# Kernel tuning notes

Measured on AMD Instinct MI355X. Metric: run time of the kernel, lower is better.

The kernel has to match this reference:

```python
import jax, jax.numpy as jnp
import numpy as np

B, N, E, H = 8, 2048, 768, 8
D = E // H  # head dim = 96


def setup_inputs() -> dict:
    key = jax.random.key(0)
    ks = jax.random.split(key, 9)
    s = 0.02
    return {
        "x": jax.random.normal(ks[0], (B, N, E), dtype=jnp.float32),
        "Wq": jax.random.normal(ks[1], (E, E), dtype=jnp.float32) * s,
        "bq": jax.random.normal(ks[2], (E,), dtype=jnp.float32) * s,
        "Wk": jax.random.normal(ks[3], (E, E), dtype=jnp.float32) * s,
        "bk": jax.random.normal(ks[4], (E,), dtype=jnp.float32) * s,
        "Wv": jax.random.normal(ks[5], (E, E), dtype=jnp.float32) * s,
        "bv": jax.random.normal(ks[6], (E,), dtype=jnp.float32) * s,
        "Wo": jax.random.normal(ks[7], (E, E), dtype=jnp.float32) * s,
        "bo": jax.random.normal(ks[8], (E,), dtype=jnp.float32) * s,
    }


def _split_heads(t):
    # [b, n, (h d)] -> [b, h, n, d]
    b, n, e = t.shape
    return t.reshape(b, n, H, D).transpose(0, 2, 1, 3)


def reference(x, Wq, bq, Wk, bk, Wv, bv, Wo, bo):
    q = _split_heads(x @ Wq + bq)
    k = _split_heads(x @ Wk + bk)
    v = _split_heads(x @ Wv + bv)
    energy = jnp.einsum("bhqd,bhkd->bhqk", q, k)
    # Faithful quirk of the source: softmax first, THEN divide by sqrt(emb_size)
    att = jax.nn.softmax(energy, axis=-1) / jnp.sqrt(jnp.float32(E))
    out = jnp.einsum("bhqk,bhkd->bhqd", att, v)
    out = out.transpose(0, 2, 1, 3).reshape(x.shape[0], x.shape[1], E)
    return out @ Wo + bo
```

## Files before the change

kernel.cpp:

```cpp
#include <hip/hip_runtime.h>
#include <hip/hip_bf16.h>
#include <stdint.h>

#define BATCH 8
#define NSEQ  2048
#define EMB   768
#define NH    8
#define HD    96

typedef unsigned short u16;
typedef __attribute__((ext_vector_type(8))) short short8;
typedef __attribute__((ext_vector_type(4))) float f32x4;
typedef __attribute__((ext_vector_type(16))) float f32x16;

static __device__ __forceinline__ u16 f2bf(float f) {
  union { float f; uint32_t u; } c{f};
  uint32_t u = c.u;
  return (u16)((u + 0x7FFFu + ((u >> 16) & 1u)) >> 16);
}

__global__ __launch_bounds__(256) void k_convert_x(const float* __restrict__ x,
                                                   u16* __restrict__ xb) {
  size_t i = ((size_t)blockIdx.x * 256 + threadIdx.x) * 8;
  float4 a = *(const float4*)(x + i);
  float4 b = *(const float4*)(x + i + 4);
  short8 o;
  o[0] = f2bf(a.x); o[1] = f2bf(a.y); o[2] = f2bf(a.z); o[3] = f2bf(a.w);
  o[4] = f2bf(b.x); o[5] = f2bf(b.y); o[6] = f2bf(b.z); o[7] = f2bf(b.w);
  *(short8*)(xb + i) = o;
}

__global__ __launch_bounds__(256) void k_wtrans(const float* __restrict__ Wq,
                                                const float* __restrict__ Wk,
                                                const float* __restrict__ Wv,
                                                const float* __restrict__ Wo,
                                                u16* __restrict__ WTall) {
  int z = blockIdx.z;
  const float* W = (z == 0) ? Wq : (z == 1) ? Wk : (z == 2) ? Wv : Wo;
  u16* WT = WTall + (size_t)z * EMB * EMB;
  __shared__ float tile[32][33];
  int o0 = blockIdx.x * 32, i0 = blockIdx.y * 32;
  int tx = threadIdx.x, ty = threadIdx.y;
#pragma unroll
  for (int r = 0; r < 4; ++r)
    tile[ty * 4 + r][tx] = W[(size_t)(i0 + ty * 4 + r) * EMB + o0 + tx];
  __syncthreads();
#pragma unroll
  for (int r = 0; r < 4; ++r)
    WT[(size_t)(o0 + ty * 4 + r) * EMB + i0 + tx] = f2bf(tile[tx][ty * 4 + r]);
}

template <bool OUTF32>
static __device__ __forceinline__ void gemm_body(const u16* __restrict__ A,
                                                 const u16* __restrict__ WT,
                                                 const float* __restrict__ bias,
                                                 void* __restrict__ out,
                                                 int m0, int n0, float oscale) {
  __shared__ u16 As[128 * 64];
  __shared__ u16 Bs[128 * 64];
  const int t = threadIdx.x;
  const int w = t >> 6, l = t & 63;
  const int lr = l & 15, lg = l >> 4;
  const int wm = (w >> 1) * 64, wn = (w & 1) * 64;
  f32x4 acc[4][4] = {};
  for (int kt = 0; kt < 12; ++kt) {
    const int k0 = kt * 64;
#pragma unroll
    for (int i = 0; i < 4; ++i) {
      int g = (w * 4 + i) * 64 + l;
      int m = g >> 3, k8 = (g & 7) * 8;
      const u16* sa = A + (size_t)(m0 + m) * EMB + k0 + k8;
      __builtin_amdgcn_global_load_lds((const __attribute__((address_space(1))) void*)sa,
                                       (__attribute__((address_space(3))) void*)&As[(w * 4 + i) * 512],
                                       16, 0, 0);
      const u16* sb = WT + (size_t)(n0 + m) * EMB + k0 + k8;
      __builtin_amdgcn_global_load_lds((const __attribute__((address_space(1))) void*)sb,
                                       (__attribute__((address_space(3))) void*)&Bs[(w * 4 + i) * 512],
                                       16, 0, 0);
    }
    __syncthreads();
#pragma unroll
    for (int ks = 0; ks < 2; ++ks) {
      short8 af[4], bfr[4];
#pragma unroll
      for (int mf = 0; mf < 4; ++mf)
        af[mf] = *(const short8*)&As[(wm + mf * 16 + lr) * 64 + ks * 32 + lg * 8];
#pragma unroll
      for (int nf = 0; nf < 4; ++nf)
        bfr[nf] = *(const short8*)&Bs[(wn + nf * 16 + lr) * 64 + ks * 32 + lg * 8];
#pragma unroll
      for (int mf = 0; mf < 4; ++mf)
#pragma unroll
        for (int nf = 0; nf < 4; ++nf)
          acc[mf][nf] = __builtin_amdgcn_mfma_f32_16x16x32_bf16(af[mf], bfr[nf], acc[mf][nf], 0, 0, 0);
    }
    __syncthreads();
  }
#pragma unroll
  for (int nf = 0; nf < 4; ++nf) {
    int col = n0 + wn + nf * 16 + lr;
    float bv = bias[col];
#pragma unroll
    for (int mf = 0; mf < 4; ++mf)
#pragma unroll
      for (int r = 0; r < 4; ++r) {
        int row = m0 + wm + mf * 16 + lg * 4 + r;
        float v = (acc[mf][nf][r] + bv) * oscale;
        if (OUTF32)
          ((float*)out)[(size_t)row * EMB + col] = v;
        else
          ((u16*)out)[(size_t)row * EMB + col] = f2bf(v);
      }
  }
}

__global__ __launch_bounds__(256) void k_qkv_gemm(const u16* __restrict__ X,
                                                  const u16* __restrict__ WTall,
                                                  const float* __restrict__ bq,
                                                  const float* __restrict__ bk,
                                                  const float* __restrict__ bv,
                                                  u16* __restrict__ Q, u16* __restrict__ K,
                                                  u16* __restrict__ V) {
  int z = blockIdx.z;
  const u16* WT = WTall + (size_t)z * EMB * EMB;
  const float* bias = (z == 0) ? bq : (z == 1) ? bk : bv;
  u16* out = (z == 0) ? Q : (z == 1) ? K : V;
  float sc = (z == 0) ? 1.4426950408889634f : 1.0f;
  gemm_body<false>(X, WT, bias, out, blockIdx.x * 128, blockIdx.y * 128, sc);
}

__global__ __launch_bounds__(256) void k_out_gemm(const u16* __restrict__ AO,
                                                  const u16* __restrict__ WTo,
                                                  const float* __restrict__ bo,
                                                  float* __restrict__ out) {
  gemm_body<true>(AO, WTo, bo, out, blockIdx.x * 128, blockIdx.y * 128, 1.0f);
}

__global__ __launch_bounds__(256) void k_vtrans(const u16* __restrict__ V,
                                                u16* __restrict__ VT) {
  const int bh = blockIdx.y, b = bh >> 3, h = bh & 7;
  const int n0 = blockIdx.x * 128;
  __shared__ u16 LT[96][136];
  const int t = threadIdx.x;
#pragma unroll
  for (int i = 0; i < 6; ++i) {
    int c = i * 256 + t;
    int n = c / 12, d8 = (c % 12) * 8;
    short8 v = *(const short8*)(V + ((size_t)(b * NSEQ + n0 + n)) * EMB + h * HD + d8);
#pragma unroll
    for (int j = 0; j < 8; ++j) LT[d8 + j][n] = (u16)v[j];
  }
  __syncthreads();
#pragma unroll
  for (int i = 0; i < 6; ++i) {
    int c = i * 256 + t;
    int d = c / 16, n8 = (c % 16) * 8;
    short8 v = *(const short8*)&LT[d][n8];
    *(short8*)(VT + ((size_t)bh * HD + d) * NSEQ + n0 + n8) = v;
  }
}

__global__ __launch_bounds__(256) void k_attn(const u16* __restrict__ Q,
                                              const u16* __restrict__ K,
                                              const u16* __restrict__ VT,
                                              u16* __restrict__ AO) {
  __shared__ u16 Ks[64][104];
  __shared__ u16 Vs[96][72];
  const int t = threadIdx.x, w = t >> 6, l = t & 63;
  const int l31 = l & 31, hi = l >> 5;
  const int bh = blockIdx.y, b = bh >> 3, h = bh & 7;
  const int q0 = blockIdx.x * 128 + w * 32;
  const size_t rowBase = (size_t)b * NSEQ;

  short8 qf[6];
#pragma unroll
  for (int ksd = 0; ksd < 6; ++ksd)
    qf[ksd] = *(const short8*)(Q + (rowBase + q0 + l31) * EMB + h * HD + ksd * 16 + hi * 8);

  f32x16 oacc[3] = {};
  float ls0 = 0.f, ls1 = 0.f, ls2 = 0.f, ls3 = 0.f;

  short8 kr[3], vr[3];
  auto load_tile = [&](int kv0) {
#pragma unroll
    for (int i = 0; i < 3; ++i) {
      int c = i * 256 + t;
      int kn = c / 12, kd8 = (c % 12) * 8;
      kr[i] = *(const short8*)(K + (rowBase + kv0 + kn) * EMB + h * HD + kd8);
      int vd = c / 8, vn8 = (c % 8) * 8;
      vr[i] = *(const short8*)(VT + ((size_t)bh * HD + vd) * NSEQ + kv0 + vn8);
    }
  };
  auto write_tile = [&]() {
#pragma unroll
    for (int i = 0; i < 3; ++i) {
      int c = i * 256 + t;
      int kn = c / 12, kd8 = (c % 12) * 8;
      *(short8*)&Ks[kn][kd8] = kr[i];
      int vd = c / 8, vn8 = (c % 8) * 8;
      *(short8*)&Vs[vd][vn8] = vr[i];
    }
  };
  load_tile(0);
  write_tile();
  __syncthreads();

  for (int tt = 0; tt < 32; ++tt) {
    if (tt < 31) load_tile((tt + 1) * 64);

    f32x16 s0 = {}, s1 = {};
    __builtin_amdgcn_s_setprio(1);
#pragma unroll
    for (int ksd = 0; ksd < 6; ++ksd) {
      short8 kf0 = *(const short8*)&Ks[l31][ksd * 16 + hi * 8];
      short8 kf1 = *(const short8*)&Ks[32 + l31][ksd * 16 + hi * 8];
      s0 = __builtin_amdgcn_mfma_f32_32x32x16_bf16(kf0, qf[ksd], s0, 0, 0, 0);
      s1 = __builtin_amdgcn_mfma_f32_32x32x16_bf16(kf1, qf[ksd], s1, 0, 0, 0);
    }
    __builtin_amdgcn_s_setprio(0);

#pragma unroll
    for (int i = 0; i < 16; i += 4) {
      float e0, e1, e2, e3, f0, f1, f2, f3;
      asm("v_exp_f32 %0, %1" : "=v"(e0) : "v"(s0[i + 0]));
      asm("v_exp_f32 %0, %1" : "=v"(e1) : "v"(s0[i + 1]));
      asm("v_exp_f32 %0, %1" : "=v"(e2) : "v"(s0[i + 2]));
      asm("v_exp_f32 %0, %1" : "=v"(e3) : "v"(s0[i + 3]));
      asm("v_exp_f32 %0, %1" : "=v"(f0) : "v"(s1[i + 0]));
      asm("v_exp_f32 %0, %1" : "=v"(f1) : "v"(s1[i + 1]));
      asm("v_exp_f32 %0, %1" : "=v"(f2) : "v"(s1[i + 2]));
      asm("v_exp_f32 %0, %1" : "=v"(f3) : "v"(s1[i + 3]));
      s0[i + 0] = e0; s0[i + 1] = e1; s0[i + 2] = e2; s0[i + 3] = e3;
      s1[i + 0] = f0; s1[i + 1] = f1; s1[i + 2] = f2; s1[i + 3] = f3;
      ls0 += e0 + e1; ls1 += e2 + e3;
      ls2 += f0 + f1; ls3 += f2 + f3;
    }

    short8 pa[4];
#pragma unroll
    for (int mt = 0; mt < 2; ++mt) {
#pragma unroll
      for (int kp = 0; kp < 2; ++kp) {
        const int rb = kp * 8;
        uint32_t w0, w1, w2, w3;
        if (mt == 0) {
          asm("v_cvt_pk_bf16_f32 %0, %1, %2" : "=v"(w0) : "v"(s0[rb + 0]), "v"(s0[rb + 1]));
          asm("v_cvt_pk_bf16_f32 %0, %1, %2" : "=v"(w1) : "v"(s0[rb + 2]), "v"(s0[rb + 3]));
          asm("v_cvt_pk_bf16_f32 %0, %1, %2" : "=v"(w2) : "v"(s0[rb + 4]), "v"(s0[rb + 5]));
          asm("v_cvt_pk_bf16_f32 %0, %1, %2" : "=v"(w3) : "v"(s0[rb + 6]), "v"(s0[rb + 7]));
        } else {
          asm("v_cvt_pk_bf16_f32 %0, %1, %2" : "=v"(w0) : "v"(s1[rb + 0]), "v"(s1[rb + 1]));
          asm("v_cvt_pk_bf16_f32 %0, %1, %2" : "=v"(w1) : "v"(s1[rb + 2]), "v"(s1[rb + 3]));
          asm("v_cvt_pk_bf16_f32 %0, %1, %2" : "=v"(w2) : "v"(s1[rb + 4]), "v"(s1[rb + 5]));
          asm("v_cvt_pk_bf16_f32 %0, %1, %2" : "=v"(w3) : "v"(s1[rb + 6]), "v"(s1[rb + 7]));
        }
        asm("v_permlane32_swap_b32 %0, %1" : "+v"(w0), "+v"(w2));
        asm("v_permlane32_swap_b32 %0, %1" : "+v"(w1), "+v"(w3));
        union { uint32_t u[4]; short8 s8; } pu;
        pu.u[0] = w0; pu.u[1] = w1; pu.u[2] = w2; pu.u[3] = w3;
        pa[mt * 2 + kp] = pu.s8;
      }
    }

    __builtin_amdgcn_s_setprio(1);
#pragma unroll
    for (int dt = 0; dt < 3; ++dt) {
#pragma unroll
      for (int ks2 = 0; ks2 < 4; ++ks2) {
        short8 vf = *(const short8*)&Vs[dt * 32 + l31][ks2 * 16 + hi * 8];
        oacc[dt] = __builtin_amdgcn_mfma_f32_32x32x16_bf16(pa[ks2], vf, oacc[dt], 0, 0, 0);
      }
    }
    __builtin_amdgcn_s_setprio(0);

    __syncthreads();
    if (tt < 31) write_tile();
    __syncthreads();
  }

  float lsum = (ls0 + ls1) + (ls2 + ls3);
  lsum += __shfl_xor(lsum, 32, 64);
  float inv = 1.0f / (lsum * 27.712812921102035f);
  float invq[16];
#pragma unroll
  for (int r = 0; r < 16; ++r)
    invq[r] = __shfl(inv, (r & 3) + 8 * (r >> 2) + 4 * hi, 64);
#pragma unroll
  for (int dt = 0; dt < 3; ++dt)
#pragma unroll
    for (int r = 0; r < 16; ++r) {
      int q = q0 + (r & 3) + 8 * (r >> 2) + 4 * hi;
      AO[(rowBase + q) * EMB + h * HD + dt * 32 + l31] = f2bf(oacc[dt][r] * invq[r]);
    }
}

extern "C" void kernel_launch(void* const* d_in, const int* in_sizes, int n_in,
                              void* d_out, int out_size, void* d_ws, size_t ws_size,
                              hipStream_t stream) {
  (void)in_sizes; (void)n_in; (void)out_size; (void)ws_size;
  const float* x  = (const float*)d_in[0];
  const float* Wq = (const float*)d_in[1];
  const float* bq = (const float*)d_in[2];
  const float* Wk = (const float*)d_in[3];
  const float* bk = (const float*)d_in[4];
  const float* Wv = (const float*)d_in[5];
  const float* bv = (const float*)d_in[6];
  const float* Wo = (const float*)d_in[7];
  const float* bo = (const float*)d_in[8];
  float* out = (float*)d_out;

  char* ws = (char*)d_ws;
  const size_t SZ = (size_t)BATCH * NSEQ * EMB * 2;
  u16* XB = (u16*)(ws);
  u16* QB = (u16*)(ws + SZ);
  u16* KB = (u16*)(ws + 2 * SZ);
  u16* VB = (u16*)(ws + 3 * SZ);
  u16* WT = (u16*)(ws + 4 * SZ);
  u16* VT = XB;
  u16* AO = VB;

  k_convert_x<<<dim3(6144), dim3(256), 0, stream>>>(x, XB);
  k_wtrans<<<dim3(24, 24, 4), dim3(32, 8), 0, stream>>>(Wq, Wk, Wv, Wo, WT);
  k_qkv_gemm<<<dim3(128, 6, 3), dim3(256), 0, stream>>>(XB, WT, bq, bk, bv, QB, KB, VB);
  k_vtrans<<<dim3(16, 64), dim3(256), 0, stream>>>(VB, VT);
  k_attn<<<dim3(16, 64), dim3(256), 0, stream>>>(QB, KB, VT, AO);
  k_out_gemm<<<dim3(128, 6), dim3(256), 0, stream>>>(AO, WT + (size_t)3 * EMB * EMB, bo, out);
}
```

Before: 293.3 us.

## Double-buffer K/V tiles and give each wave 64 query rows in attention

The attention kernel now gives each wave 64 query rows instead of 32, so every K and V fragment read from LDS feeds two MFMAs. The grid is halved to 8x64 blocks to match. K/V tiles are double-buffered in LDS with the global load issued two tiles ahead, which removes one barrier per iteration. The score computation is split into two 32-key halves so fewer score registers are live at once. The cost is higher register pressure (two Q fragment sets and six output accumulators under launch_bounds(256,2)) and fewer blocks, which may reduce occupancy and load balance across CUs.

```diff
diff --git a/kernel.cpp b/kernel.cpp
--- a/kernel.cpp
+++ b/kernel.cpp
@@ -160,25 +160,54 @@
   }
 }
 
-__global__ __launch_bounds__(256) void k_attn(const u16* __restrict__ Q,
-                                              const u16* __restrict__ K,
-                                              const u16* __restrict__ VT,
-                                              u16* __restrict__ AO) {
-  __shared__ u16 Ks[64][104];
-  __shared__ u16 Vs[96][72];
+static __device__ __forceinline__ void exp_sum(f32x16& s, float& ls) {
+#pragma unroll
+  for (int i = 0; i < 16; i += 4) {
+    float e0, e1, e2, e3;
+    asm("v_exp_f32 %0, %1" : "=v"(e0) : "v"(s[i + 0]));
+    asm("v_exp_f32 %0, %1" : "=v"(e1) : "v"(s[i + 1]));
+    asm("v_exp_f32 %0, %1" : "=v"(e2) : "v"(s[i + 2]));
+    asm("v_exp_f32 %0, %1" : "=v"(e3) : "v"(s[i + 3]));
+    s[i + 0] = e0; s[i + 1] = e1; s[i + 2] = e2; s[i + 3] = e3;
+    ls += (e0 + e1) + (e2 + e3);
+  }
+}
+
+template <int RB>
+static __device__ __forceinline__ short8 pack_pa(const f32x16& s) {
+  uint32_t w0, w1, w2, w3;
+  asm("v_cvt_pk_bf16_f32 %0, %1, %2" : "=v"(w0) : "v"(s[RB + 0]), "v"(s[RB + 1]));
+  asm("v_cvt_pk_bf16_f32 %0, %1, %2" : "=v"(w1) : "v"(s[RB + 2]), "v"(s[RB + 3]));
+  asm("v_cvt_pk_bf16_f32 %0, %1, %2" : "=v"(w2) : "v"(s[RB + 4]), "v"(s[RB + 5]));
+  asm("v_cvt_pk_bf16_f32 %0, %1, %2" : "=v"(w3) : "v"(s[RB + 6]), "v"(s[RB + 7]));
+  asm("v_permlane32_swap_b32 %0, %1" : "+v"(w0), "+v"(w2));
+  asm("v_permlane32_swap_b32 %0, %1" : "+v"(w1), "+v"(w3));
+  union { uint32_t u[4]; short8 s8; } pu;
+  pu.u[0] = w0; pu.u[1] = w1; pu.u[2] = w2; pu.u[3] = w3;
+  return pu.s8;
+}
+
+__global__ __launch_bounds__(256, 2) void k_attn(const u16* __restrict__ Q,
+                                                 const u16* __restrict__ K,
+                                                 const u16* __restrict__ VT,
+                                                 u16* __restrict__ AO) {
+  __shared__ u16 Ks[2][64][104];
+  __shared__ u16 Vs[2][96][72];
   const int t = threadIdx.x, w = t >> 6, l = t & 63;
   const int l31 = l & 31, hi = l >> 5;
   const int bh = blockIdx.y, b = bh >> 3, h = bh & 7;
-  const int q0 = blockIdx.x * 128 + w * 32;
+  const int q0 = blockIdx.x * 256 + w * 64;
   const size_t rowBase = (size_t)b * NSEQ;
 
-  short8 qf[6];
-#pragma unroll
-  for (int ksd = 0; ksd < 6; ++ksd)
-    qf[ksd] = *(const short8*)(Q + (rowBase + q0 + l31) * EMB + h * HD + ksd * 16 + hi * 8);
-
-  f32x16 oacc[3] = {};
-  float ls0 = 0.f, ls1 = 0.f, ls2 = 0.f, ls3 = 0.f;
+  short8 qf0[6], qf1[6];
+#pragma unroll
+  for (int ksd = 0; ksd < 6; ++ksd) {
+    qf0[ksd] = *(const short8*)(Q + (rowBase + q0 + l31) * EMB + h * HD + ksd * 16 + hi * 8);
+    qf1[ksd] = *(const short8*)(Q + (rowBase + q0 + 32 + l31) * EMB + h * HD + ksd * 16 + hi * 8);
+  }
+
+  f32x16 oacc0[3] = {}, oacc1[3] = {};
+  float ls0 = 0.f, ls1 = 0.f;
 
   short8 kr[3], vr[3];
   auto load_tile = [&](int kv0) {
@@ -191,107 +220,95 @@
       vr[i] = *(const short8*)(VT + ((size_t)bh * HD + vd) * NSEQ + kv0 + vn8);
     }
   };
-  auto write_tile = [&]() {
+  auto write_tile = [&](int buf) {
 #pragma unroll
     for (int i = 0; i < 3; ++i) {
       int c = i * 256 + t;
       int kn = c / 12, kd8 = (c % 12) * 8;
-      *(short8*)&Ks[kn][kd8] = kr[i];
+      *(short8*)&Ks[buf][kn][kd8] = kr[i];
       int vd = c / 8, vn8 = (c % 8) * 8;
-      *(short8*)&Vs[vd][vn8] = vr[i];
+      *(short8*)&Vs[buf][vd][vn8] = vr[i];
     }
   };
+
   load_tile(0);
-  write_tile();
+  write_tile(0);
+  load_tile(64);
   __syncthreads();
 
   for (int tt = 0; tt < 32; ++tt) {
-    if (tt < 31) load_tile((tt + 1) * 64);
-
-    f32x16 s0 = {}, s1 = {};
+    const int cur = tt & 1;
+    if (tt < 31) write_tile(cur ^ 1);
+    if (tt < 30) load_tile((tt + 2) * 64);
+
+    f32x16 s00 = {}, s01 = {};
     __builtin_amdgcn_s_setprio(1);
 #pragma unroll
     for (int ksd = 0; ksd < 6; ++ksd) {
-      short8 kf0 = *(const short8*)&Ks[l31][ksd * 16 + hi * 8];
-      short8 kf1 = *(const short8*)&Ks[32 + l31][ksd * 16 + hi * 8];
-      s0 = __builtin_amdgcn_mfma_f32_32x32x16_bf16(kf0, qf[ksd], s0, 0, 0, 0);
-      s1 = __builtin_amdgcn_mfma_f32_32x32x16_bf16(kf1, qf[ksd], s1, 0, 0, 0);
+      short8 kf = *(const short8*)&Ks[cur][l31][ksd * 16 + hi * 8];
+      s00 = __builtin_amdgcn_mfma_f32_32x32x16_bf16(kf, qf0[ksd], s00, 0, 0, 0);
+      s01 = __builtin_amdgcn_mfma_f32_32x32x16_bf16(kf, qf1[ksd], s01, 0, 0, 0);
     }
     __builtin_amdgcn_s_setprio(0);
-
-#pragma unroll
-    for (int i = 0; i < 16; i += 4) {
-      float e0, e1, e2, e3, f0, f1, f2, f3;
-      asm("v_exp_f32 %0, %1" : "=v"(e0) : "v"(s0[i + 0]));
-      asm("v_exp_f32 %0, %1" : "=v"(e1) : "v"(s0[i + 1]));
-      asm("v_exp_f32 %0, %1" : "=v"(e2) : "v"(s0[i + 2]));
-      asm("v_exp_f32 %0, %1" : "=v"(e3) : "v"(s0[i + 3]));
-      asm("v_exp_f32 %0, %1" : "=v"(f0) : "v"(s1[i + 0]));
-      asm("v_exp_f32 %0, %1" : "=v"(f1) : "v"(s1[i + 1]));
-      asm("v_exp_f32 %0, %1" : "=v"(f2) : "v"(s1[i + 2]));
-      asm("v_exp_f32 %0, %1" : "=v"(f3) : "v"(s1[i + 3]));
-      s0[i + 0] = e0; s0[i + 1] = e1; s0[i + 2] = e2; s0[i + 3] = e3;
-      s1[i + 0] = f0; s1[i + 1] = f1; s1[i + 2] = f2; s1[i + 3] = f3;
-      ls0 += e0 + e1; ls1 += e2 + e3;
-      ls2 += f0 + f1; ls3 += f2 + f3;
-    }
-
-    short8 pa[4];
-#pragma unroll
-    for (int mt = 0; mt < 2; ++mt) {
-#pragma unroll
-      for (int kp = 0; kp < 2; ++kp) {
-        const int rb = kp * 8;
-        uint32_t w0, w1, w2, w3;
-        if (mt == 0) {
-          asm("v_cvt_pk_bf16_f32 %0, %1, %2" : "=v"(w0) : "v"(s0[rb + 0]), "v"(s0[rb + 1]));
-          asm("v_cvt_pk_bf16_f32 %0, %1, %2" : "=v"(w1) : "v"(s0[rb + 2]), "v"(s0[rb + 3]));
-          asm("v_cvt_pk_bf16_f32 %0, %1, %2" : "=v"(w2) : "v"(s0[rb + 4]), "v"(s0[rb + 5]));
-          asm("v_cvt_pk_bf16_f32 %0, %1, %2" : "=v"(w3) : "v"(s0[rb + 6]), "v"(s0[rb + 7]));
-        } else {
-          asm("v_cvt_pk_bf16_f32 %0, %1, %2" : "=v"(w0) : "v"(s1[rb + 0]), "v"(s1[rb + 1]));
-          asm("v_cvt_pk_bf16_f32 %0, %1, %2" : "=v"(w1) : "v"(s1[rb + 2]), "v"(s1[rb + 3]));
-          asm("v_cvt_pk_bf16_f32 %0, %1, %2" : "=v"(w2) : "v"(s1[rb + 4]), "v"(s1[rb + 5]));
-          asm("v_cvt_pk_bf16_f32 %0, %1, %2" : "=v"(w3) : "v"(s1[rb + 6]), "v"(s1[rb + 7]));
-        }
-        asm("v_permlane32_swap_b32 %0, %1" : "+v"(w0), "+v"(w2));
-        asm("v_permlane32_swap_b32 %0, %1" : "+v"(w1), "+v"(w3));
-        union { uint32_t u[4]; short8 s8; } pu;
-        pu.u[0] = w0; pu.u[1] = w1; pu.u[2] = w2; pu.u[3] = w3;
-        pa[mt * 2 + kp] = pu.s8;
-      }
-    }
-
+    exp_sum(s00, ls0);
+    exp_sum(s01, ls1);
+    short8 paA00 = pack_pa<0>(s00), paA01 = pack_pa<8>(s00);
+    short8 paA10 = pack_pa<0>(s01), paA11 = pack_pa<8>(s01);
     __builtin_amdgcn_s_setprio(1);
 #pragma unroll
     for (int dt = 0; dt < 3; ++dt) {
-#pragma unroll
-      for (int ks2 = 0; ks2 < 4; ++ks2) {
-        short8 vf = *(const short8*)&Vs[dt * 32 + l31][ks2 * 16 + hi * 8];
-        oacc[dt] = __builtin_amdgcn_mfma_f32_32x32x16_bf16(pa[ks2], vf, oacc[dt], 0, 0, 0);
-      }
+      short8 vfa = *(const short8*)&Vs[cur][dt * 32 + l31][hi * 8];
+      short8 vfb = *(const short8*)&Vs[cur][dt * 32 + l31][16 + hi * 8];
+      oacc0[dt] = __builtin_amdgcn_mfma_f32_32x32x16_bf16(paA00, vfa, oacc0[dt], 0, 0, 0);
+      oacc1[dt] = __builtin_amdgcn_mfma_f32_32x32x16_bf16(paA10, vfa, oacc1[dt], 0, 0, 0);
+      oacc0[dt] = __builtin_amdgcn_mfma_f32_32x32x16_bf16(paA01, vfb, oacc0[dt], 0, 0, 0);
+      oacc1[dt] = __builtin_amdgcn_mfma_f32_32x32x16_bf16(paA11, vfb, oacc1[dt], 0, 0, 0);
     }
     __builtin_amdgcn_s_setprio(0);
 
+    f32x16 s10 = {}, s11 = {};
+    __builtin_amdgcn_s_setprio(1);
+#pragma unroll
+    for (int ksd = 0; ksd < 6; ++ksd) {
+      short8 kf = *(const short8*)&Ks[cur][32 + l31][ksd * 16 + hi * 8];
+      s10 = __builtin_amdgcn_mfma_f32_32x32x16_bf16(kf, qf0[ksd], s10, 0, 0, 0);
+      s11 = __builtin_amdgcn_mfma_f32_32x32x16_bf16(kf, qf1[ksd], s11, 0, 0, 0);
+    }
+    __builtin_amdgcn_s_setprio(0);
+    exp_sum(s10, ls0);
+    exp_sum(s11, ls1);
+    short8 paB00 = pack_pa<0>(s10), paB01 = pack_pa<8>(s10);
+    short8 paB10 = pack_pa<0>(s11), paB11 = pack_pa<8>(s11);
+    __builtin_amdgcn_s_setprio(1);
+#pragma unroll
+    for (int dt = 0; dt < 3; ++dt) {
+      short8 vfa = *(const short8*)&Vs[cur][dt * 32 + l31][32 + hi * 8];
+      short8 vfb = *(const short8*)&Vs[cur][dt * 32 + l31][48 + hi * 8];
+      oacc0[dt] = __builtin_amdgcn_mfma_f32_32x32x16_bf16(paB00, vfa, oacc0[dt], 0, 0, 0);
+      oacc1[dt] = __builtin_amdgcn_mfma_f32_32x32x16_bf16(paB10, vfa, oacc1[dt], 0, 0, 0);
+      oacc0[dt] = __builtin_amdgcn_mfma_f32_32x32x16_bf16(paB01, vfb, oacc0[dt], 0, 0, 0);
+      oacc1[dt] = __builtin_amdgcn_mfma_f32_32x32x16_bf16(paB11, vfb, oacc1[dt], 0, 0, 0);
+    }
+    __builtin_amdgcn_s_setprio(0);
+
     __syncthreads();
-    if (tt < 31) write_tile();
-    __syncthreads();
-  }
-
-  float lsum = (ls0 + ls1) + (ls2 + ls3);
-  lsum += __shfl_xor(lsum, 32, 64);
-  float inv = 1.0f / (lsum * 27.712812921102035f);
-  float invq[16];
-#pragma unroll
-  for (int r = 0; r < 16; ++r)
-    invq[r] = __shfl(inv, (r & 3) + 8 * (r >> 2) + 4 * hi, 64);
-#pragma unroll
-  for (int dt = 0; dt < 3; ++dt)
-#pragma unroll
-    for (int r = 0; r < 16; ++r) {
-      int q = q0 + (r & 3) + 8 * (r >> 2) + 4 * hi;
-      AO[(rowBase + q) * EMB + h * HD + dt * 32 + l31] = f2bf(oacc[dt][r] * invq[r]);
-    }
+  }
+
+  ls0 += __shfl_xor(ls0, 32, 64);
+  ls1 += __shfl_xor(ls1, 32, 64);
+  float inv0 = 1.0f / (ls0 * 27.712812921102035f);
+  float inv1 = 1.0f / (ls1 * 27.712812921102035f);
+#pragma unroll
+  for (int r = 0; r < 16; ++r) {
+    int qreg = (r & 3) + 8 * (r >> 2) + 4 * hi;
+    float iq0 = __shfl(inv0, qreg, 64);
+    float iq1 = __shfl(inv1, qreg, 64);
+#pragma unroll
+    for (int dt = 0; dt < 3; ++dt) {
+      AO[(rowBase + q0 + qreg) * EMB + h * HD + dt * 32 + l31] = f2bf(oacc0[dt][r] * iq0);
+      AO[(rowBase + q0 + 32 + qreg) * EMB + h * HD + dt * 32 + l31] = f2bf(oacc1[dt][r] * iq1);
+    }
+  }
 }
 
 extern "C" void kernel_launch(void* const* d_in, const int* in_sizes, int n_in,
@@ -323,6 +340,6 @@
   k_wtrans<<<dim3(24, 24, 4), dim3(32, 8), 0, stream>>>(Wq, Wk, Wv, Wo, WT);
   k_qkv_gemm<<<dim3(128, 6, 3), dim3(256), 0, stream>>>(XB, WT, bq, bk, bv, QB, KB, VB);
   k_vtrans<<<dim3(16, 64), dim3(256), 0, stream>>>(VB, VT);
-  k_attn<<<dim3(16, 64), dim3(256), 0, stream>>>(QB, KB, VT, AO);
+  k_attn<<<dim3(8, 64), dim3(256), 0, stream>>>(QB, KB, VT, AO);
   k_out_gemm<<<dim3(128, 6), dim3(256), 0, stream>>>(AO, WT + (size_t)3 * EMB * EMB, bo, out);
 }
```

Result: faster. 274.2 us (-6.5%).
